# Performance work log

Hardware: AMD Instinct MI355X
Metric: run time of the kernel (lower is better)

The kernel has to match this reference:

```python
import jax, jax.numpy as jnp
import numpy as np
import scipy.spatial  # needed only to replicate the module's host-side Delaunay call

V, D = 500000, 128


def setup_inputs() -> dict:
    key = jax.random.key(0)
    k1, k2 = jax.random.split(key)
    # torch: Parameter(torch.rand(V,2).logit())
    u = jax.random.uniform(k1, (V, 2), minval=1e-4, maxval=1.0 - 1e-4)
    verts_logit = jnp.log(u) - jnp.log1p(-u)
    verts_features = jax.random.uniform(k2, (V, D), dtype=jnp.float32)
    boundary = jnp.array([[-1.0, -1.0], [-1.0, 1.0], [1.0, -1.0], [1.0, 1.0]], dtype=jnp.float32)

    # Host-side Delaunay, exactly mirroring make_faces() in the torch module
    # (scipy runs in float64, same qhull options). Output shape is data-dependent,
    # so we materialize it here and pass it as an int input.
    v2 = np.asarray(verts_logit, dtype=np.float64)
    v2 = 2.0 / (1.0 + np.exp(-v2)) - 1.0  # sigmoid*2-1
    v2[:4] = np.asarray(boundary, dtype=np.float64)
    simplices = scipy.spatial.Delaunay(v2, qhull_options='i Qt Qbb Qc Qz Q12').simplices
    faces = jnp.asarray(simplices.astype(np.int64))

    return {
        'verts_logit': verts_logit,
        'verts_features': verts_features,
        'boundary': boundary,
        'faces': faces,
    }


def reference(verts_logit, verts_features, boundary, faces):
    # verts_2d = sigmoid(logit)*2 - 1, with the first 4 rows pinned to the square corners
    verts_2d = jax.nn.sigmoid(verts_logit) * 2.0 - 1.0  # (V, 2)
    verts_2d = verts_2d.at[:4].set(boundary)
    # F.pad(verts_2d, [0,1], 'constant', 1.0) -> append a column of ones
    verts_3d = jnp.pad(verts_2d, ((0, 0), (0, 1)), constant_values=1.0)  # (V, 3)
    return verts_3d, faces, verts_features
```

## Files before the change

### kernel.cpp

```cpp
#include <hip/hip_runtime.h>


__global__ void verts3d_kernel(const float* __restrict__ logit,
                               const float* __restrict__ boundary,
                               float* __restrict__ out, int V) {
    int i = blockIdx.x * blockDim.x + threadIdx.x;
    if (i >= V) return;
    float x, y;
    if (i < 4) {
        x = boundary[2 * i];
        y = boundary[2 * i + 1];
    } else {
        float lx = logit[2 * i];
        float ly = logit[2 * i + 1];
        x = 2.0f / (1.0f + expf(-lx)) - 1.0f;
        y = 2.0f / (1.0f + expf(-ly)) - 1.0f;
    }
    out[3 * i + 0] = x;
    out[3 * i + 1] = y;
    out[3 * i + 2] = 1.0f;
}

__global__ void faces_cast_kernel(const int* __restrict__ faces,
                                  float* __restrict__ out, int n) {
    int i = blockIdx.x * blockDim.x + threadIdx.x;
    if (i < n) out[i] = (float)faces[i];
}

extern "C" void kernel_launch(void* const* d_in, const int* in_sizes, int n_in,
                              void* d_out, int out_size, void* d_ws, size_t ws_size,
                              hipStream_t stream) {
    const float* verts_logit    = (const float*)d_in[0];
    const float* verts_features = (const float*)d_in[1];
    const float* boundary       = (const float*)d_in[2];
    const int*   faces          = (const int*)d_in[3];

    const int V  = in_sizes[0] / 2;
    const int nF = in_sizes[3];
    const long long featElems = (long long)in_sizes[1];

    float* out = (float*)d_out;
    float* out_verts3d  = out;
    float* out_faces    = out + (long long)3 * V;
    float* out_features = out_faces + nF;

    {
        int threads = 256;
        int blocks = (V + threads - 1) / threads;
        verts3d_kernel<<<blocks, threads, 0, stream>>>(verts_logit, boundary,
                                                       out_verts3d, V);
    }
    {
        int threads = 256;
        int blocks = (nF + threads - 1) / threads;
        faces_cast_kernel<<<blocks, threads, 0, stream>>>(faces, out_faces, nF);
    }
    hipMemcpyAsync(out_features, verts_features,
                   (size_t)featElems * sizeof(float),
                   hipMemcpyDeviceToDevice, stream);
}
```

Measured before the change: 517.8 us.

## Fuse vertex transform, face cast, and feature copy into one vectorized kernel

Replaces the two elementwise kernels and the device-to-device memcpy with a single kernel launch. Each thread handles four vertices or four faces using 128-bit loads and stores, and a grid-stride loop copies the 64M-element feature tensor with vector stores, peeled so the destination is 16-byte aligned. The goal is to remove launch overhead and make better use of bandwidth for the dominant feature copy. The source reads may be unaligned after the peel, and a hand-written copy may not match the tuned memcpy engine path.

```diff
diff --git a/kernel.cpp b/kernel.cpp
--- a/kernel.cpp
+++ b/kernel.cpp
@@ -1,30 +1,88 @@
 #include <hip/hip_runtime.h>
 
 
-__global__ void verts3d_kernel(const float* __restrict__ logit,
-                               const float* __restrict__ boundary,
-                               float* __restrict__ out, int V) {
-    int i = blockIdx.x * blockDim.x + threadIdx.x;
-    if (i >= V) return;
-    float x, y;
-    if (i < 4) {
-        x = boundary[2 * i];
-        y = boundary[2 * i + 1];
-    } else {
-        float lx = logit[2 * i];
-        float ly = logit[2 * i + 1];
-        x = 2.0f / (1.0f + expf(-lx)) - 1.0f;
-        y = 2.0f / (1.0f + expf(-ly)) - 1.0f;
+typedef float f32x4 __attribute__((ext_vector_type(4)));
+typedef int   i32x4 __attribute__((ext_vector_type(4)));
+
+__global__ __launch_bounds__(256) void fused_screen_tri(
+    const float* __restrict__ logit,
+    const float* __restrict__ feats,
+    const float* __restrict__ boundary,
+    const int*  __restrict__ faces,
+    float* __restrict__ out,
+    int V, int nF, long long nFeat)
+{
+    const long long gid      = (long long)blockIdx.x * 256 + threadIdx.x;
+    const long long nthreads = (long long)gridDim.x * 256;
+
+    float* outV = out;
+    float* outF = out + (long long)3 * V;
+    float* outX = outF + nF;
+
+    const long long W1  = (V + 3) >> 2;
+    const long long n4f = nF >> 2;
+
+    if (gid < W1) {
+        const int base = (int)gid << 2;
+        if (gid == 0) {
+            for (int v = 0; v < 4 && v < V; ++v) {
+                outV[3 * v + 0] = boundary[2 * v];
+                outV[3 * v + 1] = boundary[2 * v + 1];
+                outV[3 * v + 2] = 1.0f;
+            }
+        } else if (base + 4 <= V) {
+            f32x4 l0 = *(const f32x4*)(logit + 2 * base);
+            f32x4 l1 = *(const f32x4*)(logit + 2 * base + 4);
+            float xs[4] = { l0.x, l0.z, l1.x, l1.z };
+            float ys[4] = { l0.y, l0.w, l1.y, l1.w };
+            float o[12] __attribute__((aligned(16)));
+            #pragma unroll
+            for (int k = 0; k < 4; ++k) {
+                o[3 * k + 0] = 2.0f / (1.0f + expf(-xs[k])) - 1.0f;
+                o[3 * k + 1] = 2.0f / (1.0f + expf(-ys[k])) - 1.0f;
+                o[3 * k + 2] = 1.0f;
+            }
+            f32x4* dp = (f32x4*)(outV + 3 * base);
+            dp[0] = *(const f32x4*)&o[0];
+            dp[1] = *(const f32x4*)&o[4];
+            dp[2] = *(const f32x4*)&o[8];
+        } else {
+            for (int v = base; v < V; ++v) {
+                float sx = 2.0f / (1.0f + expf(-logit[2 * v])) - 1.0f;
+                float sy = 2.0f / (1.0f + expf(-logit[2 * v + 1])) - 1.0f;
+                outV[3 * v + 0] = sx;
+                outV[3 * v + 1] = sy;
+                outV[3 * v + 2] = 1.0f;
+            }
+        }
+    } else if (gid < W1 + n4f + 1) {
+        const long long j = gid - W1;
+        if (j < n4f) {
+            i32x4 fi = *(const i32x4*)(faces + 4 * j);
+            f32x4 fo;
+            fo.x = (float)fi.x; fo.y = (float)fi.y;
+            fo.z = (float)fi.z; fo.w = (float)fi.w;
+            *(f32x4*)(outF + 4 * j) = fo;
+        } else {
+            for (int t = (int)(n4f << 2); t < nF; ++t) outF[t] = (float)faces[t];
+        }
     }
-    out[3 * i + 0] = x;
-    out[3 * i + 1] = y;
-    out[3 * i + 2] = 1.0f;
-}
 
-__global__ void faces_cast_kernel(const int* __restrict__ faces,
-                                  float* __restrict__ out, int n) {
-    int i = blockIdx.x * blockDim.x + threadIdx.x;
-    if (i < n) out[i] = (float)faces[i];
+    int peel = (int)(((long long)3 * V + nF) & 3);
+    peel = (4 - peel) & 3;
+    if (peel > nFeat) peel = (int)nFeat;
+    if (gid < peel) outX[gid] = feats[gid];
+
+    const float* s = feats + peel;
+    float*       d = outX + peel;
+    const long long m  = nFeat - peel;
+    const long long m4 = m >> 2;
+    for (long long i = gid; i < m4; i += nthreads) {
+        f32x4 v;
+        __builtin_memcpy(&v, s + 4 * i, sizeof(v));
+        *(f32x4*)(d + 4 * i) = v;
+    }
+    for (long long i = (m4 << 2) + gid; i < m; i += nthreads) d[i] = s[i];
 }
 
 extern "C" void kernel_launch(void* const* d_in, const int* in_sizes, int n_in,
@@ -37,25 +95,16 @@
 
     const int V  = in_sizes[0] / 2;
     const int nF = in_sizes[3];
-    const long long featElems = (long long)in_sizes[1];
+    const long long nFeat = (long long)in_sizes[1];
 
-    float* out = (float*)d_out;
-    float* out_verts3d  = out;
-    float* out_faces    = out + (long long)3 * V;
-    float* out_features = out_faces + nF;
+    long long W1  = (V + 3) / 4;
+    long long n4f = nF / 4;
+    long long smallThreads = W1 + n4f + 1;
+    int blocksSmall = (int)((smallThreads + 255) / 256);
+    int blocks = 8192;
+    if (blocksSmall > blocks) blocks = blocksSmall;
 
-    {
-        int threads = 256;
-        int blocks = (V + threads - 1) / threads;
-        verts3d_kernel<<<blocks, threads, 0, stream>>>(verts_logit, boundary,
-                                                       out_verts3d, V);
-    }
-    {
-        int threads = 256;
-        int blocks = (nF + threads - 1) / threads;
-        faces_cast_kernel<<<blocks, threads, 0, stream>>>(faces, out_faces, nF);
-    }
-    hipMemcpyAsync(out_features, verts_features,
-                   (size_t)featElems * sizeof(float),
-                   hipMemcpyDeviceToDevice, stream);
+    fused_screen_tri<<<blocks, 256, 0, stream>>>(
+        verts_logit, verts_features, boundary, faces,
+        (float*)d_out, V, nF, nFeat);
 }
```

After: 456.9 us. -11.8%, faster.
